# Optimization experiments

Hardware: AMD Instinct MI355X
Metric: run time of the kernel (lower is better)

## Reference

```python
import jax, jax.numpy as jnp
import numpy as np


def conv1x1(x, w, b):
    # x: [B,C,H,W], w: [O,C], b: [O]
    return jnp.einsum('bchw,oc->bohw', x, w) + b[None, :, None, None]


def dwconv(x, w):
    # depthwise conv, x: [B,C,H,W], w: [C,1,k,k], SAME padding (k odd, pad=k//2)
    return jax.lax.conv_general_dilated(
        x, w, window_strides=(1, 1), padding='SAME',
        dimension_numbers=('NCHW', 'OIHW', 'NCHW'),
        feature_group_count=x.shape[1])


def setup_inputs() -> dict:
    key = jax.random.key(0)
    ks = jax.random.split(key, 14)
    B, C, H, W = 16, 256, 64, 64
    OC = C // 16  # scale=16 -> 16
    WSCALE = 0.05
    r = lambda k, shape: jax.random.normal(k, shape, dtype=jnp.float32) * WSCALE
    return {
        'x': jax.random.normal(ks[0], (B, C, H, W), dtype=jnp.float32),
        'conv_w': r(ks[1], (C + 4, C)),           # 1x1 conv -> ctx (C) + gates (3+1)
        'conv_b': r(ks[2], (C + 4,)),
        'fw3': r(ks[3], (C, 1, 3, 3)),            # depthwise focal kernels
        'fw5': r(ks[4], (C, 1, 5, 5)),
        'fw7': r(ks[5], (C, 1, 7, 7)),
        'key_w': r(ks[6], (1, C)),                # Conv_key 1x1
        'key_b': r(ks[7], (1,)),
        'v1_w': r(ks[8], (OC, C)),                # Conv_value first 1x1
        'v1_b': r(ks[9], (OC,)),
        'ln_w': jnp.ones((OC,), dtype=jnp.float32),
        'ln_b': jnp.zeros((OC,), dtype=jnp.float32),
        'v2_w': r(ks[10], (C, OC)),               # Conv_value second 1x1
        'v2_b': r(ks[11], (C,)),
    }


def reference(x, conv_w, conv_b, fw3, fw5, fw7, key_w, key_b,
              v1_w, v1_b, ln_w, ln_b, v2_w, v2_b):
    B, C, H, W = x.shape
    # _contextAggregation
    t = conv1x1(x, conv_w, conv_b)          # [B, C+4, H, W]
    ctx, gates = t[:, :C], t[:, C:]         # [B,C,H,W], [B,4,H,W]
    ctx_all = jnp.zeros_like(ctx)
    for l, fw in enumerate((fw3, fw5, fw7)):
        ctx = jax.nn.gelu(dwconv(ctx, fw), approximate=False)  # torch GELU = exact erf
        ctx_all = ctx_all + ctx * gates[:, l:l + 1]
    ctx_global = jnp.mean(ctx, axis=(2, 3), keepdims=True)     # AdaptiveAvgPool2d(1)
    ctx_all = ctx_all + ctx_global * gates[:, 3:4]
    # GC-style channel attention: softmax over spatial positions
    k = conv1x1(ctx_all, key_w, key_b).reshape(B, H * W)       # [B, HW]
    k = jax.nn.softmax(k, axis=1)
    q = ctx_all.reshape(B, C, H * W)
    qk = jnp.einsum('bcn,bn->bc', q, k)[:, :, None, None]      # [B,C,1,1]
    # Conv_value: 1x1 -> LayerNorm([OC,1,1]) -> ReLU -> 1x1
    v = conv1x1(qk, v1_w, v1_b)                                # [B,OC,1,1]
    mu = jnp.mean(v, axis=(1, 2, 3), keepdims=True)
    var = jnp.var(v, axis=(1, 2, 3), keepdims=True)
    v = (v - mu) * jax.lax.rsqrt(var + 1e-5)
    v = v * ln_w[None, :, None, None] + ln_b[None, :, None, None]
    v = jax.nn.relu(v)
    v = conv1x1(v, v2_w, v2_b)                                 # [B,C,1,1]
    return ctx_all + v
```

## Files before the change

kernel.cpp:

```cpp
#include <hip/hip_runtime.h>

#define DEVFN __device__ __forceinline__

constexpr int B  = 16;
constexpr int C  = 256;
constexpr int N  = 64 * 64;
constexpr int O1 = C + 4;

typedef __attribute__((ext_vector_type(8)))  short bf16x8;
typedef __attribute__((ext_vector_type(4)))  short bf16x4;
typedef __attribute__((ext_vector_type(16))) float f32x16;
typedef __attribute__((ext_vector_type(2)))  _Float16 h2;
typedef unsigned short ushort_t;
typedef unsigned int   uint32;

DEVFN short f2bf(float f){
  union { float f; unsigned u; } p; p.f = f;
  unsigned r = p.u + 0x7fffu + ((p.u >> 16) & 1u);
  return (short)(r >> 16);
}
DEVFN unsigned pack2(float lo, float hi){
  return (unsigned)(ushort_t)f2bf(lo) | ((unsigned)(ushort_t)f2bf(hi) << 16);
}
DEVFN float lo2f(unsigned u){ union{unsigned u; float f;} p; p.u = u << 16; return p.f; }
DEVFN float hi2f(unsigned u){ union{unsigned u; float f;} p; p.u = u & 0xffff0000u; return p.f; }
DEVFN float bf2f(ushort_t s){ union{unsigned u; float f;} p; p.u = (unsigned)s << 16; return p.f; }

DEVFN float gelu_fast(float x){
  float s = x * x;
  float t = x * fmaf(s, 0.1029432f, 2.3022082f);
  float e = __builtin_amdgcn_exp2f(-t);
  return x * __builtin_amdgcn_rcpf(1.0f + e);
}

DEVFN float fdot2f(uint32 a, uint32 b, float c){
#if __has_builtin(__builtin_amdgcn_fdot2)
  return __builtin_amdgcn_fdot2(__builtin_bit_cast(h2, a),
                                __builtin_bit_cast(h2, b), c, false);
#else
  h2 ha = __builtin_bit_cast(h2, a), hb = __builtin_bit_cast(h2, b);
  return fmaf((float)ha.x, (float)hb.x, fmaf((float)ha.y, (float)hb.y, c));
#endif
}

DEVFN uint32 pkh(float a, float b){
  _Float16 ha = (_Float16)a, hb = (_Float16)b;
  return (uint32)__builtin_bit_cast(ushort_t, ha) |
         ((uint32)__builtin_bit_cast(ushort_t, hb) << 16);
}

__global__ __launch_bounds__(256)
void k_wbf(const float* __restrict__ w, ushort_t* __restrict__ wbf,
           const float* __restrict__ fw3, const float* __restrict__ fw5,
           const float* __restrict__ fw7, uint32* __restrict__ w3p,
           uint32* __restrict__ w5p, uint32* __restrict__ w7p,
           const float* __restrict__ x, ushort_t* __restrict__ xbf){
  if(blockIdx.x >= 321){
    const int blk = blockIdx.x - 321;
    const int b  = blk >> 5;
    const int kg = blk & 31;
    const float* xs = x + ((size_t)(b * 256 + kg * 8)) * N;
    ushort_t* xd = xbf + ((size_t)(b * 32 + kg)) * N * 8;
    #pragma unroll
    for(int it = 0; it < 4; it++){
      const int n = (it * 256 + threadIdx.x) * 4;
      float4 cv[8];
      #pragma unroll
      for(int j = 0; j < 8; j++) cv[j] = *(const float4*)(xs + (size_t)j * N + n);
      #pragma unroll
      for(int p = 0; p < 4; p++){
        uint4 v;
        v.x = pack2(((const float*)&cv[0])[p], ((const float*)&cv[1])[p]);
        v.y = pack2(((const float*)&cv[2])[p], ((const float*)&cv[3])[p]);
        v.z = pack2(((const float*)&cv[4])[p], ((const float*)&cv[5])[p]);
        v.w = pack2(((const float*)&cv[6])[p], ((const float*)&cv[7])[p]);
        *(uint4*)(xd + (size_t)(n + p) * 8) = v;
      }
    }
    return;
  }
  if(blockIdx.x == 320){
    const int c = threadIdx.x;
    #pragma unroll
    for(int ky = 0; ky < 3; ky++){
      const float* wr = fw3 + c * 9 + ky * 3;
      w3p[c * 6 + ky * 2 + 0] = pkh(wr[0], wr[1]);
      w3p[c * 6 + ky * 2 + 1] = pkh(wr[2], 0.f);
    }
    #pragma unroll
    for(int ky = 0; ky < 5; ky++){
      const float* wr = fw5 + c * 25 + ky * 5;
      w5p[c * 15 + ky * 3 + 0] = pkh(wr[0], wr[1]);
      w5p[c * 15 + ky * 3 + 1] = pkh(wr[2], wr[3]);
      w5p[c * 15 + ky * 3 + 2] = pkh(wr[4], 0.f);
    }
    #pragma unroll
    for(int ky = 0; ky < 7; ky++){
      const float* wr = fw7 + c * 49 + ky * 7;
      w7p[c * 28 + ky * 4 + 0] = pkh(wr[0], wr[1]);
      w7p[c * 28 + ky * 4 + 1] = pkh(wr[2], wr[3]);
      w7p[c * 28 + ky * 4 + 2] = pkh(wr[4], wr[5]);
      w7p[c * 28 + ky * 4 + 3] = pkh(wr[6], 0.f);
    }
    return;
  }
  int idx = blockIdx.x * 256 + threadIdx.x;
  int o = idx >> 8, cc = idx & 255;
  wbf[idx] = (o < O1) ? (ushort_t)f2bf(w[o * 256 + cc]) : (ushort_t)0;
}

__global__ __launch_bounds__(512, 6)
void k_conv1_mfma(const ushort_t* __restrict__ xbf, const ushort_t* __restrict__ wbf,
                  const float* __restrict__ conv_w, const float* __restrict__ bias,
                  ushort_t* __restrict__ ctxb, float* __restrict__ gates){
  __shared__ __align__(16) short wlds[2][4 * 256 * 8];
  __shared__ __align__(16) short xlds[2][4 * 64 * 8];
  __shared__ float sgw[4 * 256];
  __shared__ float sbias[256];
  const int tid  = threadIdx.x;
  const int wave = tid >> 6;
  const int lane = tid & 63;
  const int l31  = lane & 31;
  const int lhi  = lane >> 5;
  const int pg   = blockIdx.x;
  const int b    = pg >> 6;
  const int n0   = (pg & 63) * 64;

  #pragma unroll
  for(int i = 0; i < 2; i++) sgw[i * 512 + tid] = conv_w[256 * 256 + i * 512 + tid];
  if(tid < 256) sbias[tid] = bias[tid];
  const int gidx = tid >> 6;
  const int gn   = tid & 63;
  float gbias = (tid < 256) ? bias[256 + gidx] : 0.f;
  float gacc = 0.f;

  f32x16 acc[2];
  #pragma unroll
  for(int t = 0; t < 2; t++)
    #pragma unroll
    for(int r = 0; r < 16; r++) acc[t][r] = 0.f;

  auto glX = [&](int kc, int bf){
    if(tid < 256){
      const int kg = tid >> 6, n = tid & 63;
      const ushort_t* src = xbf + ((size_t)(b * 32 + (kc >> 3) + kg) * N + n0 + n) * 8;
      __builtin_amdgcn_global_load_lds(
          (const __attribute__((address_space(1))) unsigned int*)src,
          (__attribute__((address_space(3))) unsigned int*)&xlds[bf][(size_t)tid * 8],
          16, 0, 0);
    }
  };
  auto glW = [&](int kc, int bf){
    #pragma unroll
    for(int q = 0; q < 2; q++){
      const int pidx = q * 512 + tid;
      const int kg = pidx >> 8;
      const int m  = pidx & 255;
      const ushort_t* src = wbf + (size_t)m * 256 + kc + kg * 8;
      __builtin_amdgcn_global_load_lds(
          (const __attribute__((address_space(1))) unsigned int*)src,
          (__attribute__((address_space(3))) unsigned int*)&wlds[bf][(size_t)pidx * 8],
          16, 0, 0);
    }
  };
  auto mfmaC = [&](int bf){
    #pragma unroll
    for(int ks = 0; ks < 2; ks++){
      const int kg = ks * 2 + lhi;
      bf16x8 af = *(const bf16x8*)&wlds[bf][(kg * 256 + wave * 32 + l31) * 8];
      bf16x8 b0 = *(const bf16x8*)&xlds[bf][(kg * 64 + l31) * 8];
      bf16x8 b1 = *(const bf16x8*)&xlds[bf][(kg * 64 + 32 + l31) * 8];
      acc[0] = __builtin_amdgcn_mfma_f32_32x32x16_bf16(af, b0, acc[0], 0, 0, 0);
      acc[1] = __builtin_amdgcn_mfma_f32_32x32x16_bf16(af, b1, acc[1], 0, 0, 0);
    }
  };
  auto gateC = [&](int bf, int kc){
    if(tid < 256){
      float a = gacc;
      #pragma unroll
      for(int kg = 0; kg < 4; kg++){
        bf16x8 xv = *(const bf16x8*)&xlds[bf][(kg * 64 + gn) * 8];
        const float* gw = &sgw[gidx * 256 + kc + kg * 8];
        #pragma unroll
        for(int j = 0; j < 4; j++){
          unsigned u = ((const unsigned*)&xv)[j];
          a = fmaf(lo2f(u), gw[2 * j], a);
          a = fmaf(hi2f(u), gw[2 * j + 1], a);
        }
      }
      gacc = a;
    }
  };

  glX(0, 0); glW(0, 0);
  __syncthreads();
  #pragma unroll
  for(int c = 0; c < 7; c++){
    const int bf = c & 1;
    glX((c + 1) * 32, bf ^ 1);
    glW((c + 1) * 32, bf ^ 1);
    mfmaC(bf);
    gateC(bf, c * 32);
    __syncthreads();
  }
  mfmaC(1);
  gateC(1, 224);

  #pragma unroll
  for(int nt = 0; nt < 2; nt++){
    const int n = n0 + nt * 32 + l31;
    #pragma unroll
    for(int r = 0; r < 16; r++){
      const int row = (r & 3) + 8 * (r >> 2) + 4 * lhi;
      const int o = wave * 32 + row;
      const float v = acc[nt][r] + sbias[o];
      _Float16 hv = (_Float16)v;
      ctxb[((size_t)(b * 256 + o)) * N + n] = __builtin_bit_cast(ushort_t, hv);
    }
  }
  if(tid < 256)
    gates[((size_t)(b * 4 + gidx)) * N + n0 + gn] = gacc + gbias;
}

constexpr int SSTR = 72;

template<int K>
DEVFN void dw_stage_dot(const short* src, const uint32* __restrict__ wp,
                        int h, int w0, float* val){
  constexpr int R = K / 2;
  constexpr int PAIRS = (K + 2) / 2;
  float acc[8];
  #pragma unroll
  for(int i = 0; i < 8; i++) acc[i] = 0.f;
  #pragma unroll
  for(int ky = 0; ky < K; ky++){
    uint32 wk[PAIRS];
    #pragma unroll
    for(int t = 0; t < PAIRS; t++) wk[t] = wp[ky * PAIRS + t];
    const int r = h + ky - R;
    if((unsigned)r < 64u){
      const short* rp = &src[r * SSTR + w0];
      uint4 a0 = *(const uint4*)rp;
      uint4 a1 = *(const uint4*)(rp + 8);
      uint32 P[8] = {a0.x, a0.y, a0.z, a0.w, a1.x, a1.y, a1.z, a1.w};
      uint32 S[7];
      #pragma unroll
      for(int j = 0; j < 7; j++)
        S[j] = __builtin_amdgcn_alignbit(P[j + 1], P[j], 16);
      #pragma unroll
      for(int i = 0; i < 8; i++){
        int j0, useP;
        if      (K == 7){ useP =  (i & 1); j0 = (i + 1) >> 1; }
        else if (K == 5){ useP = !(i & 1); j0 = (i >> 1) + 1; }
        else            { useP =  (i & 1); j0 = (i >> 1) + ((i & 1) ? 2 : 1); }
        #pragma unroll
        for(int t = 0; t < PAIRS; t++){
          const uint32 a = useP ? P[j0 + t] : S[j0 + t];
          acc[i] = fdot2f(a, wk[t], acc[i]);
        }
      }
    }
  }
  #pragma unroll
  for(int i = 0; i < 8; i++) val[i] = gelu_fast(acc[i]);
}

DEVFN void store_row_h(short* dst, int h, int w0, const float* val){
  uint32 o0 = __builtin_bit_cast(uint32, __builtin_amdgcn_cvt_pkrtz(val[0], val[1]));
  uint32 o1 = __builtin_bit_cast(uint32, __builtin_amdgcn_cvt_pkrtz(val[2], val[3]));
  uint32 o2 = __builtin_bit_cast(uint32, __builtin_amdgcn_cvt_pkrtz(val[4], val[5]));
  uint32 o3 = __builtin_bit_cast(uint32, __builtin_amdgcn_cvt_pkrtz(val[6], val[7]));
  uint2 t0; t0.x = o0; t0.y = o1;
  uint2 t1; t1.x = o2; t1.y = o3;
  *(uint2*)&dst[h * SSTR + w0 + 4] = t0;
  *(uint2*)&dst[h * SSTR + w0 + 8] = t1;
}

__global__ __launch_bounds__(512, 8)
void k_dwchain(ushort_t* __restrict__ ctxb, const uint32* __restrict__ w3p,
               const uint32* __restrict__ w5p, const uint32* __restrict__ w7p,
               const float* __restrict__ gates){
  __shared__ __align__(16) short bufA[64 * SSTR];
  __shared__ __align__(16) short bufB[64 * SSTR];
  __shared__ float wred[8];
  const int tid = threadIdx.x;
  const int plane = blockIdx.x;
  const int b = plane >> 8;
  const int c = plane & 255;
  const int h  = tid >> 3;
  const int w0 = (tid & 7) * 8;
  const int nbase = h * 64 + w0;

  if(tid < 64){
    bf16x4 z = {0, 0, 0, 0};
    *(bf16x4*)&bufA[tid * SSTR] = z;  *(bf16x4*)&bufA[tid * SSTR + 68] = z;
    *(bf16x4*)&bufB[tid * SSTR] = z;  *(bf16x4*)&bufB[tid * SSTR + 68] = z;
  }
  {
    const uint4 iv = *(const uint4*)((const short*)ctxb + (size_t)plane * N + tid * 8);
    uint2 t0; t0.x = iv.x; t0.y = iv.y;
    uint2 t1; t1.x = iv.z; t1.y = iv.w;
    *(uint2*)&bufA[h * SSTR + w0 + 4] = t0;
    *(uint2*)&bufA[h * SSTR + w0 + 8] = t1;
  }
  __syncthreads();

  float ctxp[8];
  #pragma unroll
  for(int i = 0; i < 8; i++) ctxp[i] = 0.f;
  float val[8];

  dw_stage_dot<3>(bufA, w3p + c * 6, h, w0, val);
  {
    const float* gp = gates + ((size_t)(b * 4 + 0)) * N + nbase;
    float4 ga = *(const float4*)gp, gb = *(const float4*)(gp + 4);
    ctxp[0] = fmaf(val[0], ga.x, ctxp[0]); ctxp[1] = fmaf(val[1], ga.y, ctxp[1]);
    ctxp[2] = fmaf(val[2], ga.z, ctxp[2]); ctxp[3] = fmaf(val[3], ga.w, ctxp[3]);
    ctxp[4] = fmaf(val[4], gb.x, ctxp[4]); ctxp[5] = fmaf(val[5], gb.y, ctxp[5]);
    ctxp[6] = fmaf(val[6], gb.z, ctxp[6]); ctxp[7] = fmaf(val[7], gb.w, ctxp[7]);
    store_row_h(bufB, h, w0, val);
  }
  __syncthreads();

  dw_stage_dot<5>(bufB, w5p + c * 15, h, w0, val);
  {
    const float* gp = gates + ((size_t)(b * 4 + 1)) * N + nbase;
    float4 ga = *(const float4*)gp, gb = *(const float4*)(gp + 4);
    ctxp[0] = fmaf(val[0], ga.x, ctxp[0]); ctxp[1] = fmaf(val[1], ga.y, ctxp[1]);
    ctxp[2] = fmaf(val[2], ga.z, ctxp[2]); ctxp[3] = fmaf(val[3], ga.w, ctxp[3]);
    ctxp[4] = fmaf(val[4], gb.x, ctxp[4]); ctxp[5] = fmaf(val[5], gb.y, ctxp[5]);
    ctxp[6] = fmaf(val[6], gb.z, ctxp[6]); ctxp[7] = fmaf(val[7], gb.w, ctxp[7]);
    store_row_h(bufA, h, w0, val);
  }
  __syncthreads();

  dw_stage_dot<7>(bufA, w7p + c * 28, h, w0, val);
  float lsum = 0.f;
  {
    const float* gp = gates + ((size_t)(b * 4 + 2)) * N + nbase;
    float4 ga = *(const float4*)gp, gb = *(const float4*)(gp + 4);
    ctxp[0] = fmaf(val[0], ga.x, ctxp[0]); ctxp[1] = fmaf(val[1], ga.y, ctxp[1]);
    ctxp[2] = fmaf(val[2], ga.z, ctxp[2]); ctxp[3] = fmaf(val[3], ga.w, ctxp[3]);
    ctxp[4] = fmaf(val[4], gb.x, ctxp[4]); ctxp[5] = fmaf(val[5], gb.y, ctxp[5]);
    ctxp[6] = fmaf(val[6], gb.z, ctxp[6]); ctxp[7] = fmaf(val[7], gb.w, ctxp[7]);
    #pragma unroll
    for(int i = 0; i < 8; i++) lsum += val[i];
  }
  #pragma unroll
  for(int off = 32; off > 0; off >>= 1) lsum += __shfl_xor(lsum, off, 64);
  if((tid & 63) == 0) wred[tid >> 6] = lsum;
  __syncthreads();
  float mean = 0.f;
  #pragma unroll
  for(int i = 0; i < 8; i++) mean += wred[i];
  mean *= (1.0f / 4096.0f);

  {
    const float* gp = gates + ((size_t)(b * 4 + 3)) * N + nbase;
    float4 ga = *(const float4*)gp, gb = *(const float4*)(gp + 4);
    bf16x8 ov;
    ov[0] = f2bf(fmaf(mean, ga.x, ctxp[0])); ov[1] = f2bf(fmaf(mean, ga.y, ctxp[1]));
    ov[2] = f2bf(fmaf(mean, ga.z, ctxp[2])); ov[3] = f2bf(fmaf(mean, ga.w, ctxp[3]));
    ov[4] = f2bf(fmaf(mean, gb.x, ctxp[4])); ov[5] = f2bf(fmaf(mean, gb.y, ctxp[5]));
    ov[6] = f2bf(fmaf(mean, gb.z, ctxp[6])); ov[7] = f2bf(fmaf(mean, gb.w, ctxp[7]));
    *(bf16x8*)((short*)ctxb + (size_t)plane * N + nbase) = ov;
  }
}

__global__ __launch_bounds__(256)
void k_logits(const ushort_t* __restrict__ P, const float* __restrict__ key_w,
              const float* __restrict__ key_b, float* __restrict__ logits){
  __shared__ float kw[256];
  __shared__ float part[512];
  int tid = threadIdx.x;
  kw[tid] = key_w[tid];
  __syncthreads();
  int b  = blockIdx.x >> 5;
  int n0 = (blockIdx.x & 31) * 128;
  int cpart = tid >> 6, pxp = tid & 63;
  const ushort_t* pp = P + ((size_t)(b * 256 + cpart * 64)) * N + n0 + pxp * 2;
  float a0 = 0.f, a1 = 0.f;
  #pragma unroll 8
  for(int c = 0; c < 64; c++){
    unsigned u = *(const unsigned*)(pp + (size_t)c * N);
    float kwv = kw[cpart * 64 + c];
    a0 = fmaf(lo2f(u), kwv, a0);
    a1 = fmaf(hi2f(u), kwv, a1);
  }
  part[cpart * 128 + pxp * 2]     = a0;
  part[cpart * 128 + pxp * 2 + 1] = a1;
  __syncthreads();
  if(tid < 128){
    float l = part[tid] + part[128 + tid] + part[256 + tid] + part[384 + tid];
    logits[b * N + n0 + tid] = l + key_b[0];
  }
}

__global__ __launch_bounds__(1024)
void k_softmax(float* __restrict__ kbuf){
  __shared__ float wred[16];
  int b = blockIdx.x, tid = threadIdx.x;
  const int wave = tid >> 6, lane = tid & 63;
  float v[4];
  float m = -1e30f;
  #pragma unroll
  for(int i = 0; i < 4; i++){
    v[i] = kbuf[b * N + tid + i * 1024];
    m = fmaxf(m, v[i]);
  }
  #pragma unroll
  for(int off = 32; off > 0; off >>= 1) m = fmaxf(m, __shfl_xor(m, off, 64));
  if(lane == 0) wred[wave] = m;
  __syncthreads();
  float mm = -1e30f;
  #pragma unroll
  for(int i = 0; i < 16; i++) mm = fmaxf(mm, wred[i]);
  __syncthreads();
  float s = 0.f;
  #pragma unroll
  for(int i = 0; i < 4; i++){ v[i] = __expf(v[i] - mm); s += v[i]; }
  #pragma unroll
  for(int off = 32; off > 0; off >>= 1) s += __shfl_xor(s, off, 64);
  if(lane == 0) wred[wave] = s;
  __syncthreads();
  float tot = 0.f;
  #pragma unroll
  for(int i = 0; i < 16; i++) tot += wred[i];
  float inv = 1.0f / tot;
  #pragma unroll
  for(int i = 0; i < 4; i++)
    kbuf[b * N + tid + i * 1024] = v[i] * inv;
}

__global__ __launch_bounds__(256)
void k_qk(const ushort_t* __restrict__ P, const float* __restrict__ kbuf,
          float* __restrict__ qk){
  __shared__ float red[256];
  int plane = blockIdx.x, tid = threadIdx.x;
  int b = plane >> 8;
  const unsigned* pp = (const unsigned*)(P + (size_t)plane * N);
  const float2* kp = (const float2*)(kbuf + b * N);
  float acc = 0.f;
  #pragma unroll
  for(int i = 0; i < 8; i++){
    int idx = tid + i * 256;
    unsigned u = pp[idx];
    float2 kk = kp[idx];
    acc = fmaf(lo2f(u), kk.x, acc);
    acc = fmaf(hi2f(u), kk.y, acc);
  }
  red[tid] = acc; __syncthreads();
  for(int s = 128; s > 0; s >>= 1){
    if(tid < s) red[tid] += red[tid + s];
    __syncthreads();
  }
  if(tid == 0) qk[plane] = red[0];
}

__global__ __launch_bounds__(256)
void k_v(const float* __restrict__ qk, const float* __restrict__ v1w,
         const float* __restrict__ v1b, const float* __restrict__ lnw,
         const float* __restrict__ lnb, const float* __restrict__ v2w,
         const float* __restrict__ v2b, float* __restrict__ vout){
  int b = blockIdx.x, tid = threadIdx.x;
  __shared__ float qs[256];
  __shared__ float part[256];
  __shared__ float v1s[16];
  __shared__ float vr[16];
  __shared__ float stats[2];
  qs[tid] = qk[b * 256 + tid];
  __syncthreads();
  int oc = tid >> 4, ln = tid & 15;
  float p = 0.f;
  #pragma unroll
  for(int j = 0; j < 16; j++){
    int cc = ln + j * 16;
    p = fmaf(v1w[oc * 256 + cc], qs[cc], p);
  }
  part[tid] = p;
  __syncthreads();
  if(tid < 16){
    float s = v1b[tid];
    for(int j = 0; j < 16; j++) s += part[tid * 16 + j];
    v1s[tid] = s;
  }
  __syncthreads();
  if(tid == 0){
    float mu = 0.f;
    for(int i = 0; i < 16; i++) mu += v1s[i];
    mu *= (1.f / 16.f);
    float var = 0.f;
    for(int i = 0; i < 16; i++){ float d = v1s[i] - mu; var += d * d; }
    var *= (1.f / 16.f);
    stats[0] = mu; stats[1] = rsqrtf(var + 1e-5f);
  }
  __syncthreads();
  if(tid < 16){
    float vv = (v1s[tid] - stats[0]) * stats[1] * lnw[tid] + lnb[tid];
    vr[tid] = fmaxf(vv, 0.f);
  }
  __syncthreads();
  float o = v2b[tid];
  #pragma unroll
  for(int j = 0; j < 16; j++) o = fmaf(v2w[tid * 16 + j], vr[j], o);
  vout[b * 256 + tid] = o;
}

__global__ __launch_bounds__(256)
void k_final(float* __restrict__ out, const ushort_t* __restrict__ ctxb,
             const float* __restrict__ vout){
  int idx8 = blockIdx.x * 256 + threadIdx.x;
  int plane = idx8 >> 9;
  int off = (idx8 & 511) * 8;
  bf16x8 v = *(const bf16x8*)((const short*)ctxb + (size_t)plane * N + off);
  float vv = vout[plane];
  float4 o0, o1;
  o0.x = bf2f((ushort_t)v[0]) + vv; o0.y = bf2f((ushort_t)v[1]) + vv;
  o0.z = bf2f((ushort_t)v[2]) + vv; o0.w = bf2f((ushort_t)v[3]) + vv;
  o1.x = bf2f((ushort_t)v[4]) + vv; o1.y = bf2f((ushort_t)v[5]) + vv;
  o1.z = bf2f((ushort_t)v[6]) + vv; o1.w = bf2f((ushort_t)v[7]) + vv;
  float* op = out + (size_t)plane * N + off;
  *(float4*)op = o0;
  *(float4*)(op + 4) = o1;
}

extern "C" void kernel_launch(void* const* d_in, const int* in_sizes, int n_in,
                              void* d_out, int out_size, void* d_ws, size_t ws_size,
                              hipStream_t stream){
  const float* x      = (const float*)d_in[0];
  const float* conv_w = (const float*)d_in[1];
  const float* conv_b = (const float*)d_in[2];
  const float* fw3    = (const float*)d_in[3];
  const float* fw5    = (const float*)d_in[4];
  const float* fw7    = (const float*)d_in[5];
  const float* key_w  = (const float*)d_in[6];
  const float* key_b  = (const float*)d_in[7];
  const float* v1_w   = (const float*)d_in[8];
  const float* v1_b   = (const float*)d_in[9];
  const float* ln_w   = (const float*)d_in[10];
  const float* ln_b   = (const float*)d_in[11];
  const float* v2_w   = (const float*)d_in[12];
  const float* v2_b   = (const float*)d_in[13];
  float* out = (float*)d_out;

  const size_t PL = (size_t)B * C * N;
  char* p = (char*)d_ws;
  ushort_t* ctxb = (ushort_t*)p;  p += PL * sizeof(ushort_t);
  float* gates   = (float*)p;     p += (size_t)B * 4 * N * sizeof(float);
  float* kbuf    = (float*)p;     p += (size_t)B * N * sizeof(float);
  float* qkb     = (float*)p;     p += (size_t)B * C * sizeof(float);
  float* vout    = (float*)p;     p += (size_t)B * C * sizeof(float);
  ushort_t* wbf  = (ushort_t*)p;  p += (size_t)320 * 256 * sizeof(ushort_t);
  uint32* w3p    = (uint32*)p;    p += (size_t)256 * 6 * sizeof(uint32);
  uint32* w5p    = (uint32*)p;    p += (size_t)256 * 15 * sizeof(uint32);
  uint32* w7p    = (uint32*)p;
  ushort_t* xbf  = (ushort_t*)d_out;

  k_wbf<<<833, 256, 0, stream>>>(conv_w, wbf, fw3, fw5, fw7, w3p, w5p, w7p,
                                 x, xbf);
  k_conv1_mfma<<<1024, 512, 0, stream>>>(xbf, wbf, conv_w, conv_b, ctxb, gates);
  k_dwchain<<<B * C, 512, 0, stream>>>(ctxb, w3p, w5p, w7p, gates);
  k_logits<<<512, 256, 0, stream>>>(ctxb, key_w, key_b, kbuf);
  k_softmax<<<B, 1024, 0, stream>>>(kbuf);
  k_qk<<<B * C, 256, 0, stream>>>(ctxb, kbuf, qkb);
  k_v<<<B, 256, 0, stream>>>(qkb, v1_w, v1_b, ln_w, ln_b, v2_w, v2_b, vout);
  k_final<<<8192, 256, 0, stream>>>(out, ctxb, vout);
}
```

Measured before the change: 263.0 us.

## Fuse softmax into qk reduction and value MLP into final add

Removes the separate softmax and value-MLP kernels. Each qk block now recomputes the batch's softmax max and sum from the logits and divides the dot product by the sum at the end. Each final block recomputes the small v1/LayerNorm/ReLU/v2 chain for its own channel before adding it to its slice of ctx. This drops two launches and two tiny serial kernels, at the cost of redundant per-block recomputation and an extra pass over the logits in every qk block.

New measurement: 260.3 us. Within noise of the previous version (-1.0%).

```diff
diff --git a/kernel.cpp b/kernel.cpp
--- a/kernel.cpp
+++ b/kernel.cpp
@@ -396,124 +396,108 @@
   }
 }
 
-__global__ __launch_bounds__(1024)
-void k_softmax(float* __restrict__ kbuf){
-  __shared__ float wred[16];
-  int b = blockIdx.x, tid = threadIdx.x;
+__global__ __launch_bounds__(256)
+void k_qk(const ushort_t* __restrict__ P, const float* __restrict__ logits,
+          float* __restrict__ qk){
+  __shared__ float red[256];
+  __shared__ float wred[4];
+  const int plane = blockIdx.x, tid = threadIdx.x;
+  const int b = plane >> 8;
   const int wave = tid >> 6, lane = tid & 63;
-  float v[4];
+  const float2* lp = (const float2*)(logits + b * N);
+  float2 l2[8];
   float m = -1e30f;
   #pragma unroll
-  for(int i = 0; i < 4; i++){
-    v[i] = kbuf[b * N + tid + i * 1024];
-    m = fmaxf(m, v[i]);
+  for(int i = 0; i < 8; i++){
+    l2[i] = lp[tid + i * 256];
+    m = fmaxf(m, fmaxf(l2[i].x, l2[i].y));
   }
   #pragma unroll
   for(int off = 32; off > 0; off >>= 1) m = fmaxf(m, __shfl_xor(m, off, 64));
   if(lane == 0) wred[wave] = m;
   __syncthreads();
-  float mm = -1e30f;
-  #pragma unroll
-  for(int i = 0; i < 16; i++) mm = fmaxf(mm, wred[i]);
+  m = fmaxf(fmaxf(wred[0], wred[1]), fmaxf(wred[2], wred[3]));
   __syncthreads();
   float s = 0.f;
   #pragma unroll
-  for(int i = 0; i < 4; i++){ v[i] = __expf(v[i] - mm); s += v[i]; }
+  for(int i = 0; i < 8; i++){
+    l2[i].x = __expf(l2[i].x - m);
+    l2[i].y = __expf(l2[i].y - m);
+    s += l2[i].x + l2[i].y;
+  }
   #pragma unroll
   for(int off = 32; off > 0; off >>= 1) s += __shfl_xor(s, off, 64);
   if(lane == 0) wred[wave] = s;
   __syncthreads();
-  float tot = 0.f;
-  #pragma unroll
-  for(int i = 0; i < 16; i++) tot += wred[i];
-  float inv = 1.0f / tot;
-  #pragma unroll
-  for(int i = 0; i < 4; i++)
-    kbuf[b * N + tid + i * 1024] = v[i] * inv;
+  const float stot = wred[0] + wred[1] + wred[2] + wred[3];
+  const unsigned* pp = (const unsigned*)(P + (size_t)plane * N);
+  float acc = 0.f;
+  #pragma unroll
+  for(int i = 0; i < 8; i++){
+    unsigned u = pp[tid + i * 256];
+    acc = fmaf(lo2f(u), l2[i].x, acc);
+    acc = fmaf(hi2f(u), l2[i].y, acc);
+  }
+  red[tid] = acc; __syncthreads();
+  for(int t = 128; t > 0; t >>= 1){
+    if(tid < t) red[tid] += red[tid + t];
+    __syncthreads();
+  }
+  if(tid == 0) qk[plane] = red[0] / stot;
 }
 
 __global__ __launch_bounds__(256)
-void k_qk(const ushort_t* __restrict__ P, const float* __restrict__ kbuf,
-          float* __restrict__ qk){
-  __shared__ float red[256];
-  int plane = blockIdx.x, tid = threadIdx.x;
-  int b = plane >> 8;
-  const unsigned* pp = (const unsigned*)(P + (size_t)plane * N);
-  const float2* kp = (const float2*)(kbuf + b * N);
-  float acc = 0.f;
-  #pragma unroll
-  for(int i = 0; i < 8; i++){
-    int idx = tid + i * 256;
-    unsigned u = pp[idx];
-    float2 kk = kp[idx];
-    acc = fmaf(lo2f(u), kk.x, acc);
-    acc = fmaf(hi2f(u), kk.y, acc);
-  }
-  red[tid] = acc; __syncthreads();
-  for(int s = 128; s > 0; s >>= 1){
-    if(tid < s) red[tid] += red[tid + s];
-    __syncthreads();
-  }
-  if(tid == 0) qk[plane] = red[0];
-}
-
-__global__ __launch_bounds__(256)
-void k_v(const float* __restrict__ qk, const float* __restrict__ v1w,
-         const float* __restrict__ v1b, const float* __restrict__ lnw,
-         const float* __restrict__ lnb, const float* __restrict__ v2w,
-         const float* __restrict__ v2b, float* __restrict__ vout){
-  int b = blockIdx.x, tid = threadIdx.x;
-  __shared__ float qs[256];
+void k_final(float* __restrict__ out, const ushort_t* __restrict__ ctxb,
+             const float* __restrict__ qkb, const float* __restrict__ v1w,
+             const float* __restrict__ v1b, const float* __restrict__ lnw,
+             const float* __restrict__ lnb, const float* __restrict__ v2w,
+             const float* __restrict__ v2b){
   __shared__ float part[256];
   __shared__ float v1s[16];
-  __shared__ float vr[16];
-  __shared__ float stats[2];
-  qs[tid] = qk[b * 256 + tid];
-  __syncthreads();
-  int oc = tid >> 4, ln = tid & 15;
+  __shared__ float bc[1];
+  const int tid  = threadIdx.x;
+  const int idx8 = blockIdx.x * 256 + tid;
+  const int plane = idx8 >> 9;
+  const int b = plane >> 8, c = plane & 255;
+  const int oc = tid >> 4, ln = tid & 15;
+  const float* qs = qkb + b * 256;
   float p = 0.f;
   #pragma unroll
   for(int j = 0; j < 16; j++){
-    int cc = ln + j * 16;
+    const int cc = ln + j * 16;
     p = fmaf(v1w[oc * 256 + cc], qs[cc], p);
   }
   part[tid] = p;
   __syncthreads();
   if(tid < 16){
     float s = v1b[tid];
+    #pragma unroll
     for(int j = 0; j < 16; j++) s += part[tid * 16 + j];
     v1s[tid] = s;
   }
   __syncthreads();
   if(tid == 0){
     float mu = 0.f;
+    #pragma unroll
     for(int i = 0; i < 16; i++) mu += v1s[i];
     mu *= (1.f / 16.f);
     float var = 0.f;
+    #pragma unroll
     for(int i = 0; i < 16; i++){ float d = v1s[i] - mu; var += d * d; }
     var *= (1.f / 16.f);
-    stats[0] = mu; stats[1] = rsqrtf(var + 1e-5f);
-  }
-  __syncthreads();
-  if(tid < 16){
-    float vv = (v1s[tid] - stats[0]) * stats[1] * lnw[tid] + lnb[tid];
-    vr[tid] = fmaxf(vv, 0.f);
-  }
-  __syncthreads();
-  float o = v2b[tid];
-  #pragma unroll
-  for(int j = 0; j < 16; j++) o = fmaf(v2w[tid * 16 + j], vr[j], o);
-  vout[b * 256 + tid] = o;
-}
-
-__global__ __launch_bounds__(256)
-void k_final(float* __restrict__ out, const ushort_t* __restrict__ ctxb,
-             const float* __restrict__ vout){
-  int idx8 = blockIdx.x * 256 + threadIdx.x;
-  int plane = idx8 >> 9;
-  int off = (idx8 & 511) * 8;
+    const float rs = rsqrtf(var + 1e-5f);
+    float o = v2b[c];
+    #pragma unroll
+    for(int i = 0; i < 16; i++){
+      float vv = (v1s[i] - mu) * rs * lnw[i] + lnb[i];
+      o = fmaf(v2w[c * 16 + i], fmaxf(vv, 0.f), o);
+    }
+    bc[0] = o;
+  }
+  __syncthreads();
+  const float vv = bc[0];
+  const int off = (idx8 & 511) * 8;
   bf16x8 v = *(const bf16x8*)((const short*)ctxb + (size_t)plane * N + off);
-  float vv = vout[plane];
   float4 o0, o1;
   o0.x = bf2f((ushort_t)v[0]) + vv; o0.y = bf2f((ushort_t)v[1]) + vv;
   o0.z = bf2f((ushort_t)v[2]) + vv; o0.w = bf2f((ushort_t)v[3]) + vv;
@@ -549,7 +533,6 @@
   float* gates   = (float*)p;     p += (size_t)B * 4 * N * sizeof(float);
   float* kbuf    = (float*)p;     p += (size_t)B * N * sizeof(float);
   float* qkb     = (float*)p;     p += (size_t)B * C * sizeof(float);
-  float* vout    = (float*)p;     p += (size_t)B * C * sizeof(float);
   ushort_t* wbf  = (ushort_t*)p;  p += (size_t)320 * 256 * sizeof(ushort_t);
   uint32* w3p    = (uint32*)p;    p += (size_t)256 * 6 * sizeof(uint32);
   uint32* w5p    = (uint32*)p;    p += (size_t)256 * 15 * sizeof(uint32);
@@ -561,8 +544,7 @@
   k_conv1_mfma<<<1024, 512, 0, stream>>>(xbf, wbf, conv_w, conv_b, ctxb, gates);
   k_dwchain<<<B * C, 512, 0, stream>>>(ctxb, w3p, w5p, w7p, gates);
   k_logits<<<512, 256, 0, stream>>>(ctxb, key_w, key_b, kbuf);
-  k_softmax<<<B, 1024, 0, stream>>>(kbuf);
   k_qk<<<B * C, 256, 0, stream>>>(ctxb, kbuf, qkb);
-  k_v<<<B, 256, 0, stream>>>(qkb, v1_w, v1_b, ln_w, ln_b, v2_w, v2_b, vout);
-  k_final<<<8192, 256, 0, stream>>>(out, ctxb, vout);
-}
+  k_final<<<8192, 256, 0, stream>>>(out, ctxb, qkb, v1_w, v1_b, ln_w, ln_b,
+                                    v2_w, v2_b);
+}
```
